# Kernel tuning notes

Measured on AMD Instinct MI355X. Metric: run time of the kernel, lower is better.

Reference implementation:

```python
import jax, jax.numpy as jnp
import numpy as np

NEG_SLOPE = 0.2  # PyG GATConv default negative_slope


def _gat_dense(x, W, att_src, att_dst, bias):
    """PyG GATConv on a fully-connected graph (self-loops included) == dense attention.
    x: [N, F_in], W: [F_in, H*C], att_src/att_dst: [H, C], bias: [H*C] or [C].
    Returns per-head outputs [N, H, C] (bias added by caller after concat/mean).
    """
    H, C = att_src.shape
    N = x.shape[0]
    h = (x @ W).reshape(N, H, C)                      # transformed node feats
    s = jnp.einsum('nhc,hc->nh', h, att_src)          # alpha_src per source node
    t = jnp.einsum('nhc,hc->nh', h, att_dst)          # alpha_dst per dest node
    # e[i, j, h] = leaky_relu(alpha_dst[i] + alpha_src[j]); softmax over sources j
    e = jax.nn.leaky_relu(t[:, None, :] + s[None, :, :], NEG_SLOPE)  # [N, N, H]
    a = jax.nn.softmax(e, axis=1)
    out = jnp.einsum('ijh,jhc->ihc', a, h)            # aggregate sources -> dest
    return out


def setup_inputs() -> dict:
    key = jax.random.key(0)
    ks = jax.random.split(key, 11)
    N, D, C, H = 4096, 768, 128, 4
    sd1 = 1.0 / np.sqrt(D)
    sd2 = 1.0 / np.sqrt(H * C)
    sd3 = 1.0 / np.sqrt(C)
    return {
        'node_feats': jax.random.normal(ks[0], (N, D), dtype=jnp.float32),
        'W1': jax.random.normal(ks[1], (D, H * C), dtype=jnp.float32) * sd1,
        'att_src1': jax.random.normal(ks[2], (H, C), dtype=jnp.float32) * sd3,
        'att_dst1': jax.random.normal(ks[3], (H, C), dtype=jnp.float32) * sd3,
        'b1': jnp.zeros((H * C,), dtype=jnp.float32),
        'W2': jax.random.normal(ks[4], (H * C, C), dtype=jnp.float32) * sd2,
        'att_src2': jax.random.normal(ks[5], (1, C), dtype=jnp.float32) * sd3,
        'att_dst2': jax.random.normal(ks[6], (1, C), dtype=jnp.float32) * sd3,
        'b2': jnp.zeros((C,), dtype=jnp.float32),
        'fcW': jax.random.normal(ks[7], (C, D), dtype=jnp.float32) * sd3,
        'fcb': jnp.zeros((D,), dtype=jnp.float32),
    }


def reference(node_feats, W1, att_src1, att_dst1, b1, W2, att_src2, att_dst2, b2, fcW, fcb):
    N = node_feats.shape[0]
    # GAT layer 1: 4 heads, concat=True
    x = _gat_dense(node_feats, W1, att_src1, att_dst1, b1).reshape(N, -1) + b1
    x = jax.nn.elu(x)
    # GAT layer 2: 1 head, concat=False (mean over the single head == identity)
    x = _gat_dense(x, W2, att_src2, att_dst2, b2)[:, 0, :] + b2
    x = jax.nn.elu(x)
    x = x.mean(axis=0)            # [gat_hidden]
    return x @ fcW + fcb          # [hidden_dim]
```

## Files before the change

### kernel.cpp

```cpp
#include <hip/hip_runtime.h>
#include <hip/hip_bf16.h>


#define NNODE 4096
#define CDIM 128
#define TW 132
#define NEG 0.2f
#define CHUNK 64
#define NCHUNK 64
#define SEG 8
#define SEGK (NNODE / SEG)

typedef __bf16 bf16x8 __attribute__((ext_vector_type(8)));
typedef float f32x4 __attribute__((ext_vector_type(4)));

__device__ __forceinline__ unsigned short f2b(float f) {
  unsigned int u = __float_as_uint(f);
  u += 0x7fffu + ((u >> 16) & 1u);
  return (unsigned short)(u >> 16);
}

__global__ __launch_bounds__(256) void prep_kernel(const float* __restrict__ x,
                                                   const float* __restrict__ W1,
                                                   const float* __restrict__ W2,
                                                   unsigned short* __restrict__ xb,
                                                   unsigned short* __restrict__ W1t,
                                                   unsigned short* __restrict__ W2t) {
  __shared__ float tile[64][65];
  int b = blockIdx.x, t = threadIdx.x;
  if (b < 3072) {
    int i = b * 256 + t;
    float4 v = ((const float4*)x)[i];
    ushort4 o;
    o.x = f2b(v.x); o.y = f2b(v.y); o.z = f2b(v.z); o.w = f2b(v.w);
    ((ushort4*)xb)[i] = o;
    return;
  }
  const float* W; unsigned short* Wt; int K, N, n0, k0;
  if (b < 3072 + 96) {
    int b2 = b - 3072; W = W1; Wt = W1t; K = 768; N = 512;
    n0 = (b2 & 7) * 64; k0 = (b2 >> 3) * 64;
  } else {
    int b3 = b - 3072 - 96; W = W2; Wt = W2t; K = 512; N = 128;
    n0 = (b3 & 1) * 64; k0 = (b3 >> 1) * 64;
  }
  for (int p = 0; p < 16; p++) {
    int e = p * 256 + t;
    int rr = e >> 6, cc = e & 63;
    tile[rr][cc] = W[(size_t)(k0 + rr) * N + n0 + cc];
  }
  __syncthreads();
  for (int p = 0; p < 16; p++) {
    int e = p * 256 + t;
    int rr = e >> 6, cc = e & 63;
    Wt[(size_t)(n0 + rr) * K + k0 + cc] = f2b(tile[cc][rr]);
  }
}

template <int BM, int BN>
__global__ __launch_bounds__(256) void mfma_gemm_bt(const unsigned short* __restrict__ A,
                                                    const unsigned short* __restrict__ Bt,
                                                    float* __restrict__ C,
                                                    int M, int N, int K) {
  __shared__ __align__(16) unsigned short As[BM * 40];
  __shared__ __align__(16) unsigned short Bs[BN * 40];
  constexpr int WM = BM / 2, WN = BN / 2;
  constexpr int FI = WM / 16, FJ = WN / 16;
  constexpr int EA = BM * 32 / 8;
  constexpr int EB = BN * 32 / 8;
  constexpr int NA = (EA + 255) / 256;
  constexpr int NB = (EB + 255) / 256;
  int tid = threadIdx.x;
  int lane = tid & 63, wave = tid >> 6;
  int wm = (wave >> 1) * WM, wn = (wave & 1) * WN;
  int m0 = blockIdx.y * BM, n0 = blockIdx.x * BN;
  int fm = lane & 15, fq = lane >> 4;
  f32x4 acc[FI][FJ] = {};
  for (int k0 = 0; k0 < K; k0 += 32) {
    uint4 ar[NA], br[NB];
#pragma unroll
    for (int q = 0; q < NA; q++) {
      int e = q * 256 + tid;
      if (e < EA) {
        int r = (e * 8) >> 5, kk = (e * 8) & 31;
        ar[q] = *(const uint4*)(A + (size_t)(m0 + r) * K + k0 + kk);
      }
    }
#pragma unroll
    for (int q = 0; q < NB; q++) {
      int e = q * 256 + tid;
      if (e < EB) {
        int r = (e * 8) >> 5, kk = (e * 8) & 31;
        br[q] = *(const uint4*)(Bt + (size_t)(n0 + r) * K + k0 + kk);
      }
    }
    __syncthreads();
#pragma unroll
    for (int q = 0; q < NA; q++) {
      int e = q * 256 + tid;
      if (e < EA) {
        int r = (e * 8) >> 5, kk = (e * 8) & 31;
        *(uint4*)&As[r * 40 + kk] = ar[q];
      }
    }
#pragma unroll
    for (int q = 0; q < NB; q++) {
      int e = q * 256 + tid;
      if (e < EB) {
        int r = (e * 8) >> 5, kk = (e * 8) & 31;
        *(uint4*)&Bs[r * 40 + kk] = br[q];
      }
    }
    __syncthreads();
    bf16x8 af[FI], bfr[FJ];
#pragma unroll
    for (int i = 0; i < FI; i++)
      af[i] = *(const bf16x8*)&As[(wm + i * 16 + fm) * 40 + fq * 8];
#pragma unroll
    for (int j = 0; j < FJ; j++)
      bfr[j] = *(const bf16x8*)&Bs[(wn + j * 16 + fm) * 40 + fq * 8];
#pragma unroll
    for (int i = 0; i < FI; i++)
#pragma unroll
      for (int j = 0; j < FJ; j++)
        acc[i][j] = __builtin_amdgcn_mfma_f32_16x16x32_bf16(af[i], bfr[j], acc[i][j], 0, 0, 0);
  }
#pragma unroll
  for (int i = 0; i < FI; i++) {
#pragma unroll
    for (int j = 0; j < FJ; j++) {
      int r = m0 + wm + i * 16 + fq * 4;
      int ccol = n0 + wn + j * 16 + fm;
#pragma unroll
      for (int reg = 0; reg < 4; reg++)
        C[(size_t)(r + reg) * N + ccol] = acc[i][j][reg];
    }
  }
}

__global__ void st_kernel(const float* __restrict__ h,
                          const float* __restrict__ asrc,
                          const float* __restrict__ adst,
                          float* __restrict__ s, float* __restrict__ t, int H) {
  int n = blockIdx.x;
  int wave = threadIdx.x >> 6, lane = threadIdx.x & 63;
  int HC = H * CDIM;
  float2 hv = *(const float2*)&h[(size_t)n * HC + wave * CDIM + lane * 2];
  float2 av = *(const float2*)&asrc[wave * CDIM + lane * 2];
  float2 dv = *(const float2*)&adst[wave * CDIM + lane * 2];
  float ps = hv.x * av.x + hv.y * av.y;
  float pt = hv.x * dv.x + hv.y * dv.y;
#pragma unroll
  for (int o = 32; o > 0; o >>= 1) {
    ps += __shfl_down(ps, o, 64);
    pt += __shfl_down(pt, o, 64);
  }
  if (lane == 0) {
    s[(size_t)wave * NNODE + n] = ps;
    t[(size_t)wave * NNODE + n] = pt;
  }
}

__global__ __launch_bounds__(256) void rank_count_kernel(const float* __restrict__ s,
                                                         int* __restrict__ partial) {
  __shared__ __align__(16) float keys[SEGK];
  int hh = blockIdx.z, seg = blockIdx.y, tid = threadIdx.x;
  const float* sp = s + (size_t)hh * NNODE;
  for (int k = tid; k < SEGK; k += 256) keys[k] = sp[seg * SEGK + k];
  __syncthreads();
  int mi = blockIdx.x * 256 + tid;
  float mk = sp[mi];
  int jbase = seg * SEGK;
  int cnt = 0;
#pragma unroll 4
  for (int j = 0; j < SEGK; j += 4) {
    float4 kv = *(const float4*)&keys[j];
    int jj = jbase + j;
    cnt += (kv.x < mk) || (kv.x == mk && (jj + 0) < mi);
    cnt += (kv.y < mk) || (kv.y == mk && (jj + 1) < mi);
    cnt += (kv.z < mk) || (kv.z == mk && (jj + 2) < mi);
    cnt += (kv.w < mk) || (kv.w == mk && (jj + 3) < mi);
  }
  partial[((size_t)hh * SEG + seg) * NNODE + mi] = cnt;
}

__global__ __launch_bounds__(256) void rank_scatter_kernel(const float* __restrict__ s,
                                                           const int* __restrict__ partial,
                                                           float* __restrict__ ss,
                                                           int* __restrict__ si) {
  int hh = blockIdx.y;
  int mi = blockIdx.x * 256 + threadIdx.x;
  int rank = 0;
#pragma unroll
  for (int g = 0; g < SEG; g++) rank += partial[((size_t)hh * SEG + g) * NNODE + mi];
  float mk = s[(size_t)hh * NNODE + mi];
  ss[(size_t)hh * NNODE + rank] = mk;
  si[(size_t)hh * NNODE + rank] = mi;
}

__global__ __launch_bounds__(128) void passA_kernel(const float* __restrict__ h,
                                                    const float* __restrict__ ss,
                                                    const int* __restrict__ si,
                                                    float* __restrict__ partP,
                                                    float* __restrict__ partM, int H) {
  __shared__ float eP[CHUNK], eM[CHUNK];
  __shared__ int ids[CHUNK];
  int b = blockIdx.x, hh = b / NCHUNK, ci = b % NCHUNK;
  int c = threadIdx.x;
  int HC = H * CDIM;
  int base = ci * CHUNK;
  if (c < CHUNK) {
    float sv = ss[(size_t)hh * NNODE + base + c];
    ids[c] = si[(size_t)hh * NNODE + base + c];
    eP[c] = expf(sv);
    eM[c] = expf(NEG * sv);
  }
  __syncthreads();
  float sp = 0.f, sm = 0.f;
  for (int kb = 0; kb < CHUNK; kb += 8) {
    float v[8];
#pragma unroll
    for (int j = 0; j < 8; j++)
      v[j] = h[(size_t)ids[kb + j] * HC + hh * CDIM + c];
#pragma unroll
    for (int j = 0; j < 8; j++) {
      sp = fmaf(eP[kb + j], v[j], sp);
      sm = fmaf(eM[kb + j], v[j], sm);
    }
  }
  size_t o = ((size_t)hh * NCHUNK + ci) * TW;
  partP[o + c] = sp;
  partM[o + c] = sm;
  if (c == 0) {
    float zp = 0.f, zm = 0.f;
#pragma unroll
    for (int k = 0; k < CHUNK; k++) { zp += eP[k]; zm += eM[k]; }
    partP[o + 128] = zp;
    partM[o + 128] = zm;
  }
}

__global__ __launch_bounds__(192) void passB_kernel(const float* __restrict__ partP,
                                                    const float* __restrict__ partM,
                                                    float* __restrict__ carryP,
                                                    float* __restrict__ carryM) {
  int hh = blockIdx.x, c = threadIdx.x;
  if (c > 128) return;
  float vM[NCHUNK], vP[NCHUNK];
#pragma unroll
  for (int g = 0; g < NCHUNK; g++) {
    size_t o = ((size_t)hh * NCHUNK + g) * TW + c;
    vM[g] = partM[o];
    vP[g] = partP[o];
  }
  float run = 0.f;
#pragma unroll
  for (int g = 0; g < NCHUNK; g++) {
    carryM[((size_t)hh * NCHUNK + g) * TW + c] = run;
    run += vM[g];
  }
  run = 0.f;
#pragma unroll
  for (int g = NCHUNK - 1; g >= 0; g--) {
    carryP[((size_t)hh * NCHUNK + g) * TW + c] = run;
    run += vP[g];
  }
}

__global__ __launch_bounds__(128) void passC_kernel(const float* __restrict__ h,
                                                    const float* __restrict__ ss,
                                                    const int* __restrict__ si,
                                                    const float* __restrict__ carryP,
                                                    const float* __restrict__ carryM,
                                                    float* __restrict__ SS,
                                                    float* __restrict__ PP, int H) {
  __shared__ float hrow[CHUNK][CDIM];
  __shared__ float eP[CHUNK], eM[CHUNK];
  __shared__ int ids[CHUNK];
  int b = blockIdx.x, hh = b / NCHUNK, ci = b % NCHUNK;
  int c = threadIdx.x;
  int HC = H * CDIM;
  int base = ci * CHUNK;
  size_t hb = (size_t)hh * (NNODE + 1);
  if (c < CHUNK) {
    float sv = ss[(size_t)hh * NNODE + base + c];
    ids[c] = si[(size_t)hh * NNODE + base + c];
    eP[c] = expf(sv);
    eM[c] = expf(NEG * sv);
  }
  __syncthreads();
  for (int kb = 0; kb < CHUNK; kb += 8) {
    float v[8];
#pragma unroll
    for (int j = 0; j < 8; j++)
      v[j] = h[(size_t)ids[kb + j] * HC + hh * CDIM + c];
#pragma unroll
    for (int j = 0; j < 8; j++) hrow[kb + j][c] = v[j];
  }
  size_t co = ((size_t)hh * NCHUNK + ci) * TW;
  float runm = carryM[co + c], runzm = carryM[co + 128];
#pragma unroll 8
  for (int k = 0; k < CHUNK; k++) {
    size_t row = (hb + base + k) * TW;
    PP[row + c] = runm;
    if (c == 0) PP[row + 128] = runzm;
    runm = fmaf(eM[k], hrow[k][c], runm);
    runzm += eM[k];
  }
  if (ci == NCHUNK - 1) {
    size_t row = (hb + NNODE) * TW;
    PP[row + c] = runm;
    if (c == 0) PP[row + 128] = runzm;
  }
  float runp = carryP[co + c], runzp = carryP[co + 128];
#pragma unroll 8
  for (int k = CHUNK - 1; k >= 0; k--) {
    runp = fmaf(eP[k], hrow[k][c], runp);
    runzp += eP[k];
    size_t row = (hb + base + k) * TW;
    SS[row + c] = runp;
    if (c == 0) SS[row + 128] = runzp;
  }
  if (ci == NCHUNK - 1) {
    size_t row = (hb + NNODE) * TW;
    SS[row + c] = 0.f;
    if (c == 0) SS[row + 128] = 0.f;
  }
}

template <typename OUT>
__global__ __launch_bounds__(128) void attend_kernel(const float* __restrict__ SS,
                                                     const float* __restrict__ PP,
                                                     const float* __restrict__ ss,
                                                     const float* __restrict__ tt,
                                                     const float* __restrict__ bias,
                                                     OUT* __restrict__ out, int H) {
  int b = blockIdx.x;
  int n = b / H, hh = b % H;
  int c = threadIdx.x;
  float tv = tt[(size_t)hh * NNODE + n];
  const float* sp = ss + (size_t)hh * NNODE;
  float thr = -tv;
  int lo = 0, hi = NNODE;
  while (lo < hi) { int mid = (lo + hi) >> 1; if (sp[mid] < thr) lo = mid + 1; else hi = mid; }
  size_t hb = (size_t)hh * (NNODE + 1);
  float wp = expf(tv), wm = expf(NEG * tv);
  float num = wp * SS[(hb + lo) * TW + c] + wm * PP[(hb + lo) * TW + c];
  float Z = wp * SS[(hb + lo) * TW + 128] + wm * PP[(hb + lo) * TW + 128];
  float o = num / Z + bias[hh * CDIM + c];
  float r = (o > 0.f) ? o : (expf(o) - 1.f);
  if constexpr (sizeof(OUT) == 2)
    out[(size_t)n * (H * CDIM) + hh * CDIM + c] = f2b(r);
  else
    out[(size_t)n * (H * CDIM) + hh * CDIM + c] = r;
}

__global__ __launch_bounds__(256) void mean_kernel(const float* __restrict__ x,
                                                   float* __restrict__ m) {
  __shared__ float red[256];
  int c = blockIdx.x, tid = threadIdx.x;
  float acc = 0.f;
  for (int i = tid; i < NNODE; i += 256) acc += x[(size_t)i * CDIM + c];
  red[tid] = acc; __syncthreads();
  for (int o = 128; o > 0; o >>= 1) { if (tid < o) red[tid] += red[tid + o]; __syncthreads(); }
  if (tid == 0) m[c] = red[0] * (1.f / NNODE);
}

__global__ __launch_bounds__(256) void fc_kernel(const float* __restrict__ m,
                                                 const float* __restrict__ fcW,
                                                 const float* __restrict__ fcb,
                                                 float* __restrict__ out) {
  int d = blockIdx.x * 256 + threadIdx.x;
  float acc = fcb[d];
  for (int c2 = 0; c2 < CDIM; c2++) acc = fmaf(m[c2], fcW[c2 * 768 + d], acc);
  out[d] = acc;
}

extern "C" void kernel_launch(void* const* d_in, const int* in_sizes, int n_in,
                              void* d_out, int out_size, void* d_ws, size_t ws_size,
                              hipStream_t stream) {
  const float* x   = (const float*)d_in[0];
  const float* W1  = (const float*)d_in[1];
  const float* as1 = (const float*)d_in[2];
  const float* ad1 = (const float*)d_in[3];
  const float* b1  = (const float*)d_in[4];
  const float* W2  = (const float*)d_in[5];
  const float* as2 = (const float*)d_in[6];
  const float* ad2 = (const float*)d_in[7];
  const float* b2  = (const float*)d_in[8];
  const float* fcW = (const float*)d_in[9];
  const float* fcb = (const float*)d_in[10];

  float* ws = (float*)d_ws;
  size_t off = 0;
  auto alloc = [&](size_t nfloats) { float* p = ws + off; off += nfloats; return p; };

  float* h1  = alloc((size_t)NNODE * 512);
  float* x2f = alloc((size_t)NNODE * 512);
  float* h2  = alloc((size_t)NNODE * 128);
  float* x3  = alloc((size_t)NNODE * 128);
  float* s1  = alloc((size_t)4 * NNODE);
  float* t1  = alloc((size_t)4 * NNODE);
  float* sS1 = alloc((size_t)4 * NNODE);
  int*   sI1 = (int*)alloc((size_t)4 * NNODE);
  float* SS1 = alloc((size_t)4 * (NNODE + 1) * TW);
  float* PP1 = alloc((size_t)4 * (NNODE + 1) * TW);
  float* pP1 = alloc((size_t)4 * NCHUNK * TW);
  float* pM1 = alloc((size_t)4 * NCHUNK * TW);
  float* cP1 = alloc((size_t)4 * NCHUNK * TW);
  float* cM1 = alloc((size_t)4 * NCHUNK * TW);
  float* s2  = alloc(NNODE);
  float* t2  = alloc(NNODE);
  float* sS2 = alloc(NNODE);
  int*   sI2 = (int*)alloc(NNODE);
  float* SS2 = alloc((size_t)(NNODE + 1) * TW);
  float* PP2 = alloc((size_t)(NNODE + 1) * TW);
  float* pP2 = alloc((size_t)NCHUNK * TW);
  float* pM2 = alloc((size_t)NCHUNK * TW);
  float* cP2 = alloc((size_t)NCHUNK * TW);
  float* cM2 = alloc((size_t)NCHUNK * TW);
  float* mv  = alloc(128);
  int*   rparts = (int*)alloc((size_t)4 * SEG * NNODE);

  unsigned short* xb  = (unsigned short*)PP1;
  unsigned short* W1t = (unsigned short*)SS1;
  unsigned short* x2b = (unsigned short*)x2f;
  unsigned short* W2t = (unsigned short*)(x2f + NNODE * 256 + 64);

  prep_kernel<<<3072 + 96 + 16, 256, 0, stream>>>(x, W1, W2, xb, W1t, W2t);
  mfma_gemm_bt<64, 64><<<dim3(512 / 64, NNODE / 64), 256, 0, stream>>>(xb, W1t, h1, NNODE, 512, 768);
  st_kernel<<<NNODE, 4 * 64, 0, stream>>>(h1, as1, ad1, s1, t1, 4);
  rank_count_kernel<<<dim3(NNODE / 256, SEG, 4), 256, 0, stream>>>(s1, rparts);
  rank_scatter_kernel<<<dim3(NNODE / 256, 4), 256, 0, stream>>>(s1, rparts, sS1, sI1);
  passA_kernel<<<4 * NCHUNK, 128, 0, stream>>>(h1, sS1, sI1, pP1, pM1, 4);
  passB_kernel<<<4, 192, 0, stream>>>(pP1, pM1, cP1, cM1);
  passC_kernel<<<4 * NCHUNK, 128, 0, stream>>>(h1, sS1, sI1, cP1, cM1, SS1, PP1, 4);
  attend_kernel<unsigned short><<<NNODE * 4, 128, 0, stream>>>(SS1, PP1, sS1, t1, b1, x2b, 4);
  mfma_gemm_bt<32, 64><<<dim3(128 / 64, NNODE / 32), 256, 0, stream>>>(x2b, W2t, h2, NNODE, 128, 512);
  st_kernel<<<NNODE, 1 * 64, 0, stream>>>(h2, as2, ad2, s2, t2, 1);
  rank_count_kernel<<<dim3(NNODE / 256, SEG, 1), 256, 0, stream>>>(s2, rparts);
  rank_scatter_kernel<<<dim3(NNODE / 256, 1), 256, 0, stream>>>(s2, rparts, sS2, sI2);
  passA_kernel<<<NCHUNK, 128, 0, stream>>>(h2, sS2, sI2, pP2, pM2, 1);
  passB_kernel<<<1, 192, 0, stream>>>(pP2, pM2, cP2, cM2);
  passC_kernel<<<NCHUNK, 128, 0, stream>>>(h2, sS2, sI2, cP2, cM2, SS2, PP2, 1);
  attend_kernel<float><<<NNODE, 128, 0, stream>>>(SS2, PP2, sS2, t2, b2, x3, 1);
  mean_kernel<<<128, 256, 0, stream>>>(x3, mv);
  fc_kernel<<<3, 256, 0, stream>>>(mv, fcW, fcb, (float*)d_out);
}
```

Before: 226.4 us.

## Fuse bf16 conversion into GEMM, merge rank kernels, fold carry scan into passC

Removes the separate prep kernel by converting fp32 activations and weights to bf16 inside the GEMM tile loads, with the weight transpose done on the shared-memory store. Replaces the two-kernel segmented rank count plus scatter with a single sort kernel that counts over all keys per thread. Drops passB by having each passC block compute its own prefix and suffix carries from the chunk partials. The aim is fewer launches and fewer intermediate buffers. In exchange the GEMM loads more bytes and writes Bs with scalar transposed stores, the sort does longer serial loops with fewer blocks, and passC re-reads all partials redundantly.

```diff
diff --git a/kernel.cpp b/kernel.cpp
--- a/kernel.cpp
+++ b/kernel.cpp
@@ -8,8 +8,6 @@
 #define NEG 0.2f
 #define CHUNK 64
 #define NCHUNK 64
-#define SEG 8
-#define SEGK (NNODE / SEG)
 
 typedef __bf16 bf16x8 __attribute__((ext_vector_type(8)));
 typedef float f32x4 __attribute__((ext_vector_type(4)));
@@ -19,57 +17,23 @@
   u += 0x7fffu + ((u >> 16) & 1u);
   return (unsigned short)(u >> 16);
 }
-
-__global__ __launch_bounds__(256) void prep_kernel(const float* __restrict__ x,
-                                                   const float* __restrict__ W1,
-                                                   const float* __restrict__ W2,
-                                                   unsigned short* __restrict__ xb,
-                                                   unsigned short* __restrict__ W1t,
-                                                   unsigned short* __restrict__ W2t) {
-  __shared__ float tile[64][65];
-  int b = blockIdx.x, t = threadIdx.x;
-  if (b < 3072) {
-    int i = b * 256 + t;
-    float4 v = ((const float4*)x)[i];
-    ushort4 o;
-    o.x = f2b(v.x); o.y = f2b(v.y); o.z = f2b(v.z); o.w = f2b(v.w);
-    ((ushort4*)xb)[i] = o;
-    return;
-  }
-  const float* W; unsigned short* Wt; int K, N, n0, k0;
-  if (b < 3072 + 96) {
-    int b2 = b - 3072; W = W1; Wt = W1t; K = 768; N = 512;
-    n0 = (b2 & 7) * 64; k0 = (b2 >> 3) * 64;
-  } else {
-    int b3 = b - 3072 - 96; W = W2; Wt = W2t; K = 512; N = 128;
-    n0 = (b3 & 1) * 64; k0 = (b3 >> 1) * 64;
-  }
-  for (int p = 0; p < 16; p++) {
-    int e = p * 256 + t;
-    int rr = e >> 6, cc = e & 63;
-    tile[rr][cc] = W[(size_t)(k0 + rr) * N + n0 + cc];
-  }
-  __syncthreads();
-  for (int p = 0; p < 16; p++) {
-    int e = p * 256 + t;
-    int rr = e >> 6, cc = e & 63;
-    Wt[(size_t)(n0 + rr) * K + k0 + cc] = f2b(tile[cc][rr]);
-  }
-}
-
-template <int BM, int BN>
-__global__ __launch_bounds__(256) void mfma_gemm_bt(const unsigned short* __restrict__ A,
-                                                    const unsigned short* __restrict__ Bt,
-                                                    float* __restrict__ C,
-                                                    int M, int N, int K) {
+__device__ __forceinline__ unsigned int pack2(float a, float b) {
+  return (unsigned int)f2b(a) | ((unsigned int)f2b(b) << 16);
+}
+
+template <int BM, int BN, bool A_BF16>
+__global__ __launch_bounds__(256) void mfma_gemm(const void* __restrict__ Ap,
+                                                 const float* __restrict__ B,
+                                                 float* __restrict__ C,
+                                                 int M, int N, int K) {
   __shared__ __align__(16) unsigned short As[BM * 40];
   __shared__ __align__(16) unsigned short Bs[BN * 40];
   constexpr int WM = BM / 2, WN = BN / 2;
   constexpr int FI = WM / 16, FJ = WN / 16;
   constexpr int EA = BM * 32 / 8;
-  constexpr int EB = BN * 32 / 8;
   constexpr int NA = (EA + 255) / 256;
-  constexpr int NB = (EB + 255) / 256;
+  constexpr int EBF = 32 * BN / 4;
+  constexpr int NBF = (EBF + 255) / 256;
   int tid = threadIdx.x;
   int lane = tid & 63, wave = tid >> 6;
   int wm = (wave >> 1) * WM, wn = (wave & 1) * WN;
@@ -77,21 +41,29 @@
   int fm = lane & 15, fq = lane >> 4;
   f32x4 acc[FI][FJ] = {};
   for (int k0 = 0; k0 < K; k0 += 32) {
-    uint4 ar[NA], br[NB];
+    uint4 ar[NA];
+    float4 bw[NBF];
 #pragma unroll
     for (int q = 0; q < NA; q++) {
       int e = q * 256 + tid;
       if (e < EA) {
-        int r = (e * 8) >> 5, kk = (e * 8) & 31;
-        ar[q] = *(const uint4*)(A + (size_t)(m0 + r) * K + k0 + kk);
-      }
-    }
-#pragma unroll
-    for (int q = 0; q < NB; q++) {
+        int r = e >> 2, kk = (e & 3) * 8;
+        if constexpr (A_BF16) {
+          ar[q] = *(const uint4*)((const unsigned short*)Ap + (size_t)(m0 + r) * K + k0 + kk);
+        } else {
+          const float4* pa = (const float4*)((const float*)Ap + (size_t)(m0 + r) * K + k0 + kk);
+          float4 f0 = pa[0], f1 = pa[1];
+          ar[q].x = pack2(f0.x, f0.y); ar[q].y = pack2(f0.z, f0.w);
+          ar[q].z = pack2(f1.x, f1.y); ar[q].w = pack2(f1.z, f1.w);
+        }
+      }
+    }
+#pragma unroll
+    for (int q = 0; q < NBF; q++) {
       int e = q * 256 + tid;
-      if (e < EB) {
-        int r = (e * 8) >> 5, kk = (e * 8) & 31;
-        br[q] = *(const uint4*)(Bt + (size_t)(n0 + r) * K + k0 + kk);
+      if (e < EBF) {
+        int kk = e / (BN / 4), n4 = e % (BN / 4);
+        bw[q] = *(const float4*)(B + (size_t)(k0 + kk) * N + n0 + n4 * 4);
       }
     }
     __syncthreads();
@@ -99,16 +71,19 @@
     for (int q = 0; q < NA; q++) {
       int e = q * 256 + tid;
       if (e < EA) {
-        int r = (e * 8) >> 5, kk = (e * 8) & 31;
+        int r = e >> 2, kk = (e & 3) * 8;
         *(uint4*)&As[r * 40 + kk] = ar[q];
       }
     }
 #pragma unroll
-    for (int q = 0; q < NB; q++) {
+    for (int q = 0; q < NBF; q++) {
       int e = q * 256 + tid;
-      if (e < EB) {
-        int r = (e * 8) >> 5, kk = (e * 8) & 31;
-        *(uint4*)&Bs[r * 40 + kk] = br[q];
+      if (e < EBF) {
+        int kk = e / (BN / 4), n4 = e % (BN / 4);
+        Bs[(n4 * 4 + 0) * 40 + kk] = f2b(bw[q].x);
+        Bs[(n4 * 4 + 1) * 40 + kk] = f2b(bw[q].y);
+        Bs[(n4 * 4 + 2) * 40 + kk] = f2b(bw[q].z);
+        Bs[(n4 * 4 + 3) * 40 + kk] = f2b(bw[q].w);
       }
     }
     __syncthreads();
@@ -161,41 +136,28 @@
   }
 }
 
-__global__ __launch_bounds__(256) void rank_count_kernel(const float* __restrict__ s,
-                                                         int* __restrict__ partial) {
-  __shared__ __align__(16) float keys[SEGK];
-  int hh = blockIdx.z, seg = blockIdx.y, tid = threadIdx.x;
+__global__ __launch_bounds__(256) void sort_kernel(const float* __restrict__ s,
+                                                   float* __restrict__ ss,
+                                                   int* __restrict__ si) {
+  __shared__ __align__(16) float keys[NNODE];
+  int hh = blockIdx.y, mib = blockIdx.x, tid = threadIdx.x;
   const float* sp = s + (size_t)hh * NNODE;
-  for (int k = tid; k < SEGK; k += 256) keys[k] = sp[seg * SEGK + k];
+  for (int k4 = tid; k4 < NNODE / 4; k4 += 256)
+    ((float4*)keys)[k4] = ((const float4*)sp)[k4];
   __syncthreads();
-  int mi = blockIdx.x * 256 + tid;
-  float mk = sp[mi];
-  int jbase = seg * SEGK;
+  int mi = mib * 256 + tid;
+  float mk = keys[mi];
   int cnt = 0;
 #pragma unroll 4
-  for (int j = 0; j < SEGK; j += 4) {
+  for (int j = 0; j < NNODE; j += 4) {
     float4 kv = *(const float4*)&keys[j];
-    int jj = jbase + j;
-    cnt += (kv.x < mk) || (kv.x == mk && (jj + 0) < mi);
-    cnt += (kv.y < mk) || (kv.y == mk && (jj + 1) < mi);
-    cnt += (kv.z < mk) || (kv.z == mk && (jj + 2) < mi);
-    cnt += (kv.w < mk) || (kv.w == mk && (jj + 3) < mi);
-  }
-  partial[((size_t)hh * SEG + seg) * NNODE + mi] = cnt;
-}
-
-__global__ __launch_bounds__(256) void rank_scatter_kernel(const float* __restrict__ s,
-                                                           const int* __restrict__ partial,
-                                                           float* __restrict__ ss,
-                                                           int* __restrict__ si) {
-  int hh = blockIdx.y;
-  int mi = blockIdx.x * 256 + threadIdx.x;
-  int rank = 0;
-#pragma unroll
-  for (int g = 0; g < SEG; g++) rank += partial[((size_t)hh * SEG + g) * NNODE + mi];
-  float mk = s[(size_t)hh * NNODE + mi];
-  ss[(size_t)hh * NNODE + rank] = mk;
-  si[(size_t)hh * NNODE + rank] = mi;
+    cnt += (kv.x < mk) || (kv.x == mk && (j + 0) < mi);
+    cnt += (kv.y < mk) || (kv.y == mk && (j + 1) < mi);
+    cnt += (kv.z < mk) || (kv.z == mk && (j + 2) < mi);
+    cnt += (kv.w < mk) || (kv.w == mk && (j + 3) < mi);
+  }
+  ss[(size_t)hh * NNODE + cnt] = mk;
+  si[(size_t)hh * NNODE + cnt] = mi;
 }
 
 __global__ __launch_bounds__(128) void passA_kernel(const float* __restrict__ h,
@@ -240,38 +202,11 @@
   }
 }
 
-__global__ __launch_bounds__(192) void passB_kernel(const float* __restrict__ partP,
-                                                    const float* __restrict__ partM,
-                                                    float* __restrict__ carryP,
-                                                    float* __restrict__ carryM) {
-  int hh = blockIdx.x, c = threadIdx.x;
-  if (c > 128) return;
-  float vM[NCHUNK], vP[NCHUNK];
-#pragma unroll
-  for (int g = 0; g < NCHUNK; g++) {
-    size_t o = ((size_t)hh * NCHUNK + g) * TW + c;
-    vM[g] = partM[o];
-    vP[g] = partP[o];
-  }
-  float run = 0.f;
-#pragma unroll
-  for (int g = 0; g < NCHUNK; g++) {
-    carryM[((size_t)hh * NCHUNK + g) * TW + c] = run;
-    run += vM[g];
-  }
-  run = 0.f;
-#pragma unroll
-  for (int g = NCHUNK - 1; g >= 0; g--) {
-    carryP[((size_t)hh * NCHUNK + g) * TW + c] = run;
-    run += vP[g];
-  }
-}
-
 __global__ __launch_bounds__(128) void passC_kernel(const float* __restrict__ h,
                                                     const float* __restrict__ ss,
                                                     const int* __restrict__ si,
-                                                    const float* __restrict__ carryP,
-                                                    const float* __restrict__ carryM,
+                                                    const float* __restrict__ partP,
+                                                    const float* __restrict__ partM,
                                                     float* __restrict__ SS,
                                                     float* __restrict__ PP, int H) {
   __shared__ float hrow[CHUNK][CDIM];
@@ -289,6 +224,38 @@
     eM[c] = expf(NEG * sv);
   }
   __syncthreads();
+  float cm = 0.f, cp = 0.f;
+  for (int g0 = 0; g0 < NCHUNK; g0 += 16) {
+    float vm[16], vp[16];
+#pragma unroll
+    for (int j = 0; j < 16; j++) {
+      size_t o = ((size_t)hh * NCHUNK + g0 + j) * TW + c;
+      vm[j] = partM[o];
+      vp[j] = partP[o];
+    }
+#pragma unroll
+    for (int j = 0; j < 16; j++) {
+      if (g0 + j < ci) cm += vm[j];
+      if (g0 + j > ci) cp += vp[j];
+    }
+  }
+  float zcm = 0.f, zcp = 0.f;
+  if (c == 0) {
+    for (int g0 = 0; g0 < NCHUNK; g0 += 16) {
+      float vm[16], vp[16];
+#pragma unroll
+      for (int j = 0; j < 16; j++) {
+        size_t o = ((size_t)hh * NCHUNK + g0 + j) * TW + 128;
+        vm[j] = partM[o];
+        vp[j] = partP[o];
+      }
+#pragma unroll
+      for (int j = 0; j < 16; j++) {
+        if (g0 + j < ci) zcm += vm[j];
+        if (g0 + j > ci) zcp += vp[j];
+      }
+    }
+  }
   for (int kb = 0; kb < CHUNK; kb += 8) {
     float v[8];
 #pragma unroll
@@ -297,8 +264,7 @@
 #pragma unroll
     for (int j = 0; j < 8; j++) hrow[kb + j][c] = v[j];
   }
-  size_t co = ((size_t)hh * NCHUNK + ci) * TW;
-  float runm = carryM[co + c], runzm = carryM[co + 128];
+  float runm = cm, runzm = zcm;
 #pragma unroll 8
   for (int k = 0; k < CHUNK; k++) {
     size_t row = (hb + base + k) * TW;
@@ -312,7 +278,7 @@
     PP[row + c] = runm;
     if (c == 0) PP[row + 128] = runzm;
   }
-  float runp = carryP[co + c], runzp = carryP[co + 128];
+  float runp = cp, runzp = zcp;
 #pragma unroll 8
   for (int k = CHUNK - 1; k >= 0; k--) {
     runp = fmaf(eP[k], hrow[k][c], runp);
@@ -396,7 +362,7 @@
   auto alloc = [&](size_t nfloats) { float* p = ws + off; off += nfloats; return p; };
 
   float* h1  = alloc((size_t)NNODE * 512);
-  float* x2f = alloc((size_t)NNODE * 512);
+  float* x2f = alloc((size_t)NNODE * 256);
   float* h2  = alloc((size_t)NNODE * 128);
   float* x3  = alloc((size_t)NNODE * 128);
   float* s1  = alloc((size_t)4 * NNODE);
@@ -407,8 +373,6 @@
   float* PP1 = alloc((size_t)4 * (NNODE + 1) * TW);
   float* pP1 = alloc((size_t)4 * NCHUNK * TW);
   float* pM1 = alloc((size_t)4 * NCHUNK * TW);
-  float* cP1 = alloc((size_t)4 * NCHUNK * TW);
-  float* cM1 = alloc((size_t)4 * NCHUNK * TW);
   float* s2  = alloc(NNODE);
   float* t2  = alloc(NNODE);
   float* sS2 = alloc(NNODE);
@@ -417,32 +381,21 @@
   float* PP2 = alloc((size_t)(NNODE + 1) * TW);
   float* pP2 = alloc((size_t)NCHUNK * TW);
   float* pM2 = alloc((size_t)NCHUNK * TW);
-  float* cP2 = alloc((size_t)NCHUNK * TW);
-  float* cM2 = alloc((size_t)NCHUNK * TW);
   float* mv  = alloc(128);
-  int*   rparts = (int*)alloc((size_t)4 * SEG * NNODE);
-
-  unsigned short* xb  = (unsigned short*)PP1;
-  unsigned short* W1t = (unsigned short*)SS1;
+
   unsigned short* x2b = (unsigned short*)x2f;
-  unsigned short* W2t = (unsigned short*)(x2f + NNODE * 256 + 64);
-
-  prep_kernel<<<3072 + 96 + 16, 256, 0, stream>>>(x, W1, W2, xb, W1t, W2t);
-  mfma_gemm_bt<64, 64><<<dim3(512 / 64, NNODE / 64), 256, 0, stream>>>(xb, W1t, h1, NNODE, 512, 768);
+
+  mfma_gemm<64, 64, false><<<dim3(512 / 64, NNODE / 64), 256, 0, stream>>>(x, W1, h1, NNODE, 512, 768);
   st_kernel<<<NNODE, 4 * 64, 0, stream>>>(h1, as1, ad1, s1, t1, 4);
-  rank_count_kernel<<<dim3(NNODE / 256, SEG, 4), 256, 0, stream>>>(s1, rparts);
-  rank_scatter_kernel<<<dim3(NNODE / 256, 4), 256, 0, stream>>>(s1, rparts, sS1, sI1);
+  sort_kernel<<<dim3(NNODE / 256, 4), 256, 0, stream>>>(s1, sS1, sI1);
   passA_kernel<<<4 * NCHUNK, 128, 0, stream>>>(h1, sS1, sI1, pP1, pM1, 4);
-  passB_kernel<<<4, 192, 0, stream>>>(pP1, pM1, cP1, cM1);
-  passC_kernel<<<4 * NCHUNK, 128, 0, stream>>>(h1, sS1, sI1, cP1, cM1, SS1, PP1, 4);
+  passC_kernel<<<4 * NCHUNK, 128, 0, stream>>>(h1, sS1, sI1, pP1, pM1, SS1, PP1, 4);
   attend_kernel<unsigned short><<<NNODE * 4, 128, 0, stream>>>(SS1, PP1, sS1, t1, b1, x2b, 4);
-  mfma_gemm_bt<32, 64><<<dim3(128 / 64, NNODE / 32), 256, 0, stream>>>(x2b, W2t, h2, NNODE, 128, 512);
+  mfma_gemm<32, 64, true><<<dim3(128 / 64, NNODE / 32), 256, 0, stream>>>(x2b, W2, h2, NNODE, 128, 512);
   st_kernel<<<NNODE, 1 * 64, 0, stream>>>(h2, as2, ad2, s2, t2, 1);
-  rank_count_kernel<<<dim3(NNODE / 256, SEG, 1), 256, 0, stream>>>(s2, rparts);
-  rank_scatter_kernel<<<dim3(NNODE / 256, 1), 256, 0, stream>>>(s2, rparts, sS2, sI2);
+  sort_kernel<<<dim3(NNODE / 256, 1), 256, 0, stream>>>(s2, sS2, sI2);
   passA_kernel<<<NCHUNK, 128, 0, stream>>>(h2, sS2, sI2, pP2, pM2, 1);
-  passB_kernel<<<1, 192, 0, stream>>>(pP2, pM2, cP2, cM2);
-  passC_kernel<<<NCHUNK, 128, 0, stream>>>(h2, sS2, sI2, cP2, cM2, SS2, PP2, 1);
+  passC_kernel<<<NCHUNK, 128, 0, stream>>>(h2, sS2, sI2, pP2, pM2, SS2, PP2, 1);
   attend_kernel<float><<<NNODE, 128, 0, stream>>>(SS2, PP2, sS2, t2, b2, x3, 1);
   mean_kernel<<<128, 256, 0, stream>>>(x3, mv);
   fc_kernel<<<3, 256, 0, stream>>>(mv, fcW, fcb, (float*)d_out);
```

Result: slower. 412.9 us (+82.3%).

## Prefetch next GEMM k-tile into registers and fold carry scan into passC

Applied to the files above, without the earlier changes.

The MFMA GEMM now loads the next k-slice from global memory into registers while the current slice is being multiplied, so load latency overlaps compute. The separate passB prefix-scan kernel is removed. Each passC block now sums the chunk partials before and after itself directly, which saves two kernel launches and the carry buffers. In exchange, every passC block re-reads all 64 chunk partials, adding redundant global reads.

```diff
diff --git a/kernel.cpp b/kernel.cpp
--- a/kernel.cpp
+++ b/kernel.cpp
@@ -76,42 +76,60 @@
   int m0 = blockIdx.y * BM, n0 = blockIdx.x * BN;
   int fm = lane & 15, fq = lane >> 4;
   f32x4 acc[FI][FJ] = {};
+  uint4 ar[NA], br[NB];
+#pragma unroll
+  for (int q = 0; q < NA; q++) {
+    int e = q * 256 + tid;
+    if (e < EA) {
+      int r = e >> 2, kk = (e & 3) * 8;
+      ar[q] = *(const uint4*)(A + (size_t)(m0 + r) * K + kk);
+    }
+  }
+#pragma unroll
+  for (int q = 0; q < NB; q++) {
+    int e = q * 256 + tid;
+    if (e < EB) {
+      int r = e >> 2, kk = (e & 3) * 8;
+      br[q] = *(const uint4*)(Bt + (size_t)(n0 + r) * K + kk);
+    }
+  }
   for (int k0 = 0; k0 < K; k0 += 32) {
-    uint4 ar[NA], br[NB];
+    __syncthreads();
 #pragma unroll
     for (int q = 0; q < NA; q++) {
       int e = q * 256 + tid;
       if (e < EA) {
-        int r = (e * 8) >> 5, kk = (e * 8) & 31;
-        ar[q] = *(const uint4*)(A + (size_t)(m0 + r) * K + k0 + kk);
+        int r = e >> 2, kk = (e & 3) * 8;
+        *(uint4*)&As[r * 40 + kk] = ar[q];
       }
     }
 #pragma unroll
     for (int q = 0; q < NB; q++) {
       int e = q * 256 + tid;
       if (e < EB) {
-        int r = (e * 8) >> 5, kk = (e * 8) & 31;
-        br[q] = *(const uint4*)(Bt + (size_t)(n0 + r) * K + k0 + kk);
+        int r = e >> 2, kk = (e & 3) * 8;
+        *(uint4*)&Bs[r * 40 + kk] = br[q];
       }
     }
     __syncthreads();
-#pragma unroll
-    for (int q = 0; q < NA; q++) {
-      int e = q * 256 + tid;
-      if (e < EA) {
-        int r = (e * 8) >> 5, kk = (e * 8) & 31;
-        *(uint4*)&As[r * 40 + kk] = ar[q];
-      }
-    }
-#pragma unroll
-    for (int q = 0; q < NB; q++) {
-      int e = q * 256 + tid;
-      if (e < EB) {
-        int r = (e * 8) >> 5, kk = (e * 8) & 31;
-        *(uint4*)&Bs[r * 40 + kk] = br[q];
-      }
-    }
-    __syncthreads();
+    if (k0 + 32 < K) {
+#pragma unroll
+      for (int q = 0; q < NA; q++) {
+        int e = q * 256 + tid;
+        if (e < EA) {
+          int r = e >> 2, kk = (e & 3) * 8;
+          ar[q] = *(const uint4*)(A + (size_t)(m0 + r) * K + k0 + 32 + kk);
+        }
+      }
+#pragma unroll
+      for (int q = 0; q < NB; q++) {
+        int e = q * 256 + tid;
+        if (e < EB) {
+          int r = e >> 2, kk = (e & 3) * 8;
+          br[q] = *(const uint4*)(Bt + (size_t)(n0 + r) * K + k0 + 32 + kk);
+        }
+      }
+    }
     bf16x8 af[FI], bfr[FJ];
 #pragma unroll
     for (int i = 0; i < FI; i++)
@@ -193,8 +211,7 @@
   int rank = 0;
 #pragma unroll
   for (int g = 0; g < SEG; g++) rank += partial[((size_t)hh * SEG + g) * NNODE + mi];
-  float mk = s[(size_t)hh * NNODE + mi];
-  ss[(size_t)hh * NNODE + rank] = mk;
+  ss[(size_t)hh * NNODE + rank] = s[(size_t)hh * NNODE + mi];
   si[(size_t)hh * NNODE + rank] = mi;
 }
 
@@ -240,38 +257,11 @@
   }
 }
 
-__global__ __launch_bounds__(192) void passB_kernel(const float* __restrict__ partP,
-                                                    const float* __restrict__ partM,
-                                                    float* __restrict__ carryP,
-                                                    float* __restrict__ carryM) {
-  int hh = blockIdx.x, c = threadIdx.x;
-  if (c > 128) return;
-  float vM[NCHUNK], vP[NCHUNK];
-#pragma unroll
-  for (int g = 0; g < NCHUNK; g++) {
-    size_t o = ((size_t)hh * NCHUNK + g) * TW + c;
-    vM[g] = partM[o];
-    vP[g] = partP[o];
-  }
-  float run = 0.f;
-#pragma unroll
-  for (int g = 0; g < NCHUNK; g++) {
-    carryM[((size_t)hh * NCHUNK + g) * TW + c] = run;
-    run += vM[g];
-  }
-  run = 0.f;
-#pragma unroll
-  for (int g = NCHUNK - 1; g >= 0; g--) {
-    carryP[((size_t)hh * NCHUNK + g) * TW + c] = run;
-    run += vP[g];
-  }
-}
-
 __global__ __launch_bounds__(128) void passC_kernel(const float* __restrict__ h,
                                                     const float* __restrict__ ss,
                                                     const int* __restrict__ si,
-                                                    const float* __restrict__ carryP,
-                                                    const float* __restrict__ carryM,
+                                                    const float* __restrict__ partP,
+                                                    const float* __restrict__ partM,
                                                     float* __restrict__ SS,
                                                     float* __restrict__ PP, int H) {
   __shared__ float hrow[CHUNK][CDIM];
@@ -289,6 +279,38 @@
     eM[c] = expf(NEG * sv);
   }
   __syncthreads();
+  float cm = 0.f, cp = 0.f;
+  for (int g0 = 0; g0 < NCHUNK; g0 += 16) {
+    float vm[16], vp[16];
+#pragma unroll
+    for (int j = 0; j < 16; j++) {
+      size_t o = ((size_t)hh * NCHUNK + g0 + j) * TW + c;
+      vm[j] = partM[o];
+      vp[j] = partP[o];
+    }
+#pragma unroll
+    for (int j = 0; j < 16; j++) {
+      if (g0 + j < ci) cm += vm[j];
+      if (g0 + j > ci) cp += vp[j];
+    }
+  }
+  float zcm = 0.f, zcp = 0.f;
+  if (c == 0) {
+    for (int g0 = 0; g0 < NCHUNK; g0 += 16) {
+      float vm[16], vp[16];
+#pragma unroll
+      for (int j = 0; j < 16; j++) {
+        size_t o = ((size_t)hh * NCHUNK + g0 + j) * TW + 128;
+        vm[j] = partM[o];
+        vp[j] = partP[o];
+      }
+#pragma unroll
+      for (int j = 0; j < 16; j++) {
+        if (g0 + j < ci) zcm += vm[j];
+        if (g0 + j > ci) zcp += vp[j];
+      }
+    }
+  }
   for (int kb = 0; kb < CHUNK; kb += 8) {
     float v[8];
 #pragma unroll
@@ -297,8 +319,7 @@
 #pragma unroll
     for (int j = 0; j < 8; j++) hrow[kb + j][c] = v[j];
   }
-  size_t co = ((size_t)hh * NCHUNK + ci) * TW;
-  float runm = carryM[co + c], runzm = carryM[co + 128];
+  float runm = cm, runzm = zcm;
 #pragma unroll 8
   for (int k = 0; k < CHUNK; k++) {
     size_t row = (hb + base + k) * TW;
@@ -312,7 +333,7 @@
     PP[row + c] = runm;
     if (c == 0) PP[row + 128] = runzm;
   }
-  float runp = carryP[co + c], runzp = carryP[co + 128];
+  float runp = cp, runzp = zcp;
 #pragma unroll 8
   for (int k = CHUNK - 1; k >= 0; k--) {
     runp = fmaf(eP[k], hrow[k][c], runp);
@@ -396,7 +417,7 @@
   auto alloc = [&](size_t nfloats) { float* p = ws + off; off += nfloats; return p; };
 
   float* h1  = alloc((size_t)NNODE * 512);
-  float* x2f = alloc((size_t)NNODE * 512);
+  float* x2f = alloc((size_t)NNODE * 256 + 64 + 16384);
   float* h2  = alloc((size_t)NNODE * 128);
   float* x3  = alloc((size_t)NNODE * 128);
   float* s1  = alloc((size_t)4 * NNODE);
@@ -407,8 +428,6 @@
   float* PP1 = alloc((size_t)4 * (NNODE + 1) * TW);
   float* pP1 = alloc((size_t)4 * NCHUNK * TW);
   float* pM1 = alloc((size_t)4 * NCHUNK * TW);
-  float* cP1 = alloc((size_t)4 * NCHUNK * TW);
-  float* cM1 = alloc((size_t)4 * NCHUNK * TW);
   float* s2  = alloc(NNODE);
   float* t2  = alloc(NNODE);
   float* sS2 = alloc(NNODE);
@@ -417,8 +436,6 @@
   float* PP2 = alloc((size_t)(NNODE + 1) * TW);
   float* pP2 = alloc((size_t)NCHUNK * TW);
   float* pM2 = alloc((size_t)NCHUNK * TW);
-  float* cP2 = alloc((size_t)NCHUNK * TW);
-  float* cM2 = alloc((size_t)NCHUNK * TW);
   float* mv  = alloc(128);
   int*   rparts = (int*)alloc((size_t)4 * SEG * NNODE);
 
@@ -433,16 +450,14 @@
   rank_count_kernel<<<dim3(NNODE / 256, SEG, 4), 256, 0, stream>>>(s1, rparts);
   rank_scatter_kernel<<<dim3(NNODE / 256, 4), 256, 0, stream>>>(s1, rparts, sS1, sI1);
   passA_kernel<<<4 * NCHUNK, 128, 0, stream>>>(h1, sS1, sI1, pP1, pM1, 4);
-  passB_kernel<<<4, 192, 0, stream>>>(pP1, pM1, cP1, cM1);
-  passC_kernel<<<4 * NCHUNK, 128, 0, stream>>>(h1, sS1, sI1, cP1, cM1, SS1, PP1, 4);
+  passC_kernel<<<4 * NCHUNK, 128, 0, stream>>>(h1, sS1, sI1, pP1, pM1, SS1, PP1, 4);
   attend_kernel<unsigned short><<<NNODE * 4, 128, 0, stream>>>(SS1, PP1, sS1, t1, b1, x2b, 4);
   mfma_gemm_bt<32, 64><<<dim3(128 / 64, NNODE / 32), 256, 0, stream>>>(x2b, W2t, h2, NNODE, 128, 512);
   st_kernel<<<NNODE, 1 * 64, 0, stream>>>(h2, as2, ad2, s2, t2, 1);
   rank_count_kernel<<<dim3(NNODE / 256, SEG, 1), 256, 0, stream>>>(s2, rparts);
   rank_scatter_kernel<<<dim3(NNODE / 256, 1), 256, 0, stream>>>(s2, rparts, sS2, sI2);
   passA_kernel<<<NCHUNK, 128, 0, stream>>>(h2, sS2, sI2, pP2, pM2, 1);
-  passB_kernel<<<1, 192, 0, stream>>>(pP2, pM2, cP2, cM2);
-  passC_kernel<<<NCHUNK, 128, 0, stream>>>(h2, sS2, sI2, cP2, cM2, SS2, PP2, 1);
+  passC_kernel<<<NCHUNK, 128, 0, stream>>>(h2, sS2, sI2, pP2, pM2, SS2, PP2, 1);
   attend_kernel<float><<<NNODE, 128, 0, stream>>>(SS2, PP2, sS2, t2, b2, x3, 1);
   mean_kernel<<<128, 256, 0, stream>>>(x3, mv);
   fc_kernel<<<3, 256, 0, stream>>>(mv, fcW, fcb, (float*)d_out);
```

Result: no change. 224.9 us (-0.7%).
